# Performance work log

Measured on AMD Instinct MI355X. Metric: run time of the kernel, lower is better.

Reference implementation:

```python
import jax, jax.numpy as jnp
import numpy as np

B, T, C = 2, 2048, 1024
H, DH = 16, 64          # n_heads = d_model // 64
WIN = 256               # sliding window size
K = 32                  # n_oscillators
DFF = 4096              # d_ff_hidden
NEG = -1e9


def setup_inputs() -> dict:
    key = jax.random.key(0)
    ks = jax.random.split(key, 16)
    sC = 1.0 / np.sqrt(C)
    sF = 1.0 / np.sqrt(DFF)
    sK = 1.0 / np.sqrt(K)
    return {
        "x": jax.random.normal(ks[0], (B, T, C), jnp.float32),
        "norm1_w": jnp.ones((C,), jnp.float32),
        "qkv_w": jax.random.normal(ks[1], (3 * C, C), jnp.float32) * sC,
        "qkv_b": jnp.zeros((3 * C,), jnp.float32),
        "proj_w": jax.random.normal(ks[2], (C, C), jnp.float32) * sC,
        "proj_b": jnp.zeros((C,), jnp.float32),
        "gate_w": jax.random.normal(ks[3], (1, C), jnp.float32) * 0.01,
        "gate_b": jnp.zeros((1,), jnp.float32),
        "trn_win": jax.random.normal(ks[4], (K, C), jnp.float32) * sC,
        "trn_wout": jax.random.normal(ks[5], (C, K), jnp.float32) * sK,
        "trn_gate_w": jax.random.normal(ks[6], (K, C), jnp.float32) * sC,
        "trn_gate_b": jnp.zeros((K,), jnp.float32),
        "trn_a_logit": jax.random.normal(ks[7], (K,), jnp.float32),
        "trn_theta": jax.random.uniform(ks[8], (K,), jnp.float32, 0.0, np.pi),
        "trn_res_scale": jnp.asarray(0.1, jnp.float32),
        "norm2_w": jnp.ones((C,), jnp.float32),
        "ffn_gate_w": jax.random.normal(ks[9], (DFF, C), jnp.float32) * sC,
        "ffn_up_w": jax.random.normal(ks[10], (DFF, C), jnp.float32) * sC,
        "ffn_down_w": jax.random.normal(ks[11], (C, DFF), jnp.float32) * sF,
    }


def _rms(z, w, eps=1e-6):
    return z * jax.lax.rsqrt(jnp.mean(z * z, axis=-1, keepdims=True) + eps) * w


def reference(x, norm1_w, qkv_w, qkv_b, proj_w, proj_b, gate_w, gate_b,
              trn_win, trn_wout, trn_gate_w, trn_gate_b, trn_a_logit,
              trn_theta, trn_res_scale, norm2_w, ffn_gate_w, ffn_up_w,
              ffn_down_w):
    h = _rms(x, norm1_w)

    # ---- windowed causal attention (dense mask, as in the original) ----
    qkv = h @ qkv_w.T + qkv_b                       # [B,T,3C]
    q, k, v = jnp.split(qkv, 3, axis=-1)
    heads = lambda t: t.reshape(B, T, H, DH).transpose(0, 2, 1, 3)  # [B,H,T,DH]
    q, k, v = heads(q), heads(k), heads(v)
    row = jnp.arange(T)[:, None]
    col = jnp.arange(T)[None, :]
    mask = jnp.where((col <= row) & (col >= row - WIN + 1), 0.0, NEG).astype(x.dtype)
    scores = jnp.einsum('bhqd,bhkd->bhqk', q, k) / jnp.sqrt(jnp.asarray(DH, x.dtype))
    attn = jax.nn.softmax(scores + mask, axis=-1)
    ao = jnp.einsum('bhqk,bhkd->bhqd', attn, v).transpose(0, 2, 1, 3).reshape(B, T, C)
    ao = ao @ proj_w.T + proj_b

    # ---- temporal resonance branch: K damped rotating oscillators ----
    u = h @ trn_win.T                               # [B,T,K] drive
    a = jax.nn.sigmoid(trn_a_logit)                 # amplitude in (0,1) (amplitude_max=1)
    ct, st = jnp.cos(trn_theta), jnp.sin(trn_theta)

    def step(carry, ut):
        sr, si = carry
        nsr = a * (ct * sr - st * si) + ut
        nsi = a * (st * sr + ct * si)
        return (nsr, nsi), nsr

    init = (jnp.zeros((B, K), x.dtype), jnp.zeros((B, K), x.dtype))
    _, ys = jax.lax.scan(step, init, u.transpose(1, 0, 2))  # ys: [T,B,K]
    y = ys.transpose(1, 0, 2)                                # [B,T,K]
    tg = jax.nn.sigmoid(h @ trn_gate_w.T + trn_gate_b)
    trn_out = ((tg * y) @ trn_wout.T) * trn_res_scale        # [B,T,C]

    # ---- sigmoid gate mix + residual ----
    g = jax.nn.sigmoid(h @ gate_w.T + gate_b)       # [B,T,1]
    x = x + g * ao + (1.0 - g) * trn_out

    # ---- SwiGLU FFN ----
    h2 = _rms(x, norm2_w)
    ffn = (jax.nn.silu(h2 @ ffn_gate_w.T) * (h2 @ ffn_up_w.T)) @ ffn_down_w.T
    return x + ffn
```

## Files before the change

kernel.cpp:

```cpp
#include <hip/hip_runtime.h>


typedef unsigned short u16;
typedef unsigned short u16x8 __attribute__((ext_vector_type(8)));
typedef __bf16 bf16x8 __attribute__((ext_vector_type(8)));
typedef float f32x4 __attribute__((ext_vector_type(4)));

#define DI static __device__ __forceinline__

DI u16 f2b(float f){
  union { float f; unsigned u; } v; v.f = f;
  unsigned r = v.u + 0x7FFFu + ((v.u >> 16) & 1u);
  return (u16)(r >> 16);
}
DI float b2f(u16 b){
  union { unsigned u; float f; } v; v.u = ((unsigned)b) << 16; return v.f;
}
DI u16x8 ld8(const u16* p){ return *(const u16x8*)p; }

DI f32x4 MFMA16(u16x8 a, u16x8 b, f32x4 c){
  return __builtin_amdgcn_mfma_f32_16x16x32_bf16(
      __builtin_bit_cast(bf16x8, a), __builtin_bit_cast(bf16x8, b), c, 0, 0, 0);
}

DI void async16(const void* g, void* l){
  void* gg = const_cast<void*>(g);
  __builtin_amdgcn_global_load_lds(
      (__attribute__((address_space(1))) void*)gg,
      (__attribute__((address_space(3))) void*)l, 16, 0, 0);
}

__global__ __launch_bounds__(256) void convert_w(
    const float* __restrict__ qkvw, const float* __restrict__ projw,
    const float* __restrict__ fgw, const float* __restrict__ fuw,
    const float* __restrict__ fdw, const float* __restrict__ twin,
    const float* __restrict__ tgw, const float* __restrict__ twout,
    u16* __restrict__ dst)
{
  size_t i = (size_t)blockIdx.x * 256 + threadIdx.x;
  if (i >= 4235264u) return;
  size_t e = i * 4;
  float4 v;
  if (e < 3145728u)        v = *(const float4*)(qkvw + e);
  else if (e < 3276800u){
    size_t i2 = e - 3145728u;
    int row = (int)(i2 >> 10), c = (int)(i2 & 1023);
    if (row < 32)      v = *(const float4*)(twin + row * 1024 + c);
    else if (row < 64) v = *(const float4*)(tgw + (row - 32) * 1024 + c);
    else               v = make_float4(0.f, 0.f, 0.f, 0.f);
  }
  else if (e < 4325376u)   v = *(const float4*)(projw + (e - 3276800u));
  else if (e < 12713984u){
    size_t i2 = e - 4325376u;
    int row = (int)(i2 >> 10), c = (int)(i2 & 1023);
    int G = row >> 5, j = row & 31;
    const float* src = (j < 16) ? fgw : fuw;
    v = *(const float4*)(src + (size_t)(G * 16 + (j & 15)) * 1024 + c);
  }
  else if (e < 16908288u)  v = *(const float4*)(fdw + (e - 12713984u));
  else                     v = *(const float4*)(twout + (e - 16908288u));
  uint2 p;
  p.x = (unsigned)f2b(v.x) | ((unsigned)f2b(v.y) << 16);
  p.y = (unsigned)f2b(v.z) | ((unsigned)f2b(v.w) << 16);
  *(uint2*)(dst + e) = p;
}

__global__ __launch_bounds__(256) void rmsnorm_gate(
    const float* __restrict__ x, const float* __restrict__ w,
    const float* __restrict__ gw, const float* __restrict__ gb,
    u16* __restrict__ h, float* __restrict__ g)
{
  const int row = blockIdx.x, tid = threadIdx.x;
  const int wave = tid >> 6, lane = tid & 63;
  __shared__ float sb[8];
  float4 xv = ((const float4*)(x + (size_t)row * 1024))[tid];
  float ss = xv.x*xv.x + xv.y*xv.y + xv.z*xv.z + xv.w*xv.w;
#pragma unroll
  for (int m = 32; m; m >>= 1) ss += __shfl_xor(ss, m);
  if (lane == 0) sb[wave] = ss;
  __syncthreads();
  float rstd = rsqrtf((sb[0]+sb[1]+sb[2]+sb[3]) * (1.f/1024.f) + 1e-6f);
  float4 wv = ((const float4*)w)[tid];
  float h0 = xv.x*rstd*wv.x, h1 = xv.y*rstd*wv.y;
  float h2v = xv.z*rstd*wv.z, h3 = xv.w*rstd*wv.w;
  uint2 pk;
  pk.x = (unsigned)f2b(h0) | ((unsigned)f2b(h1) << 16);
  pk.y = (unsigned)f2b(h2v) | ((unsigned)f2b(h3) << 16);
  ((uint2*)(h + (size_t)row * 1024))[tid] = pk;
  float4 gv = ((const float4*)gw)[tid];
  float gd = h0*gv.x + h1*gv.y + h2v*gv.z + h3*gv.w;
#pragma unroll
  for (int m = 32; m; m >>= 1) gd += __shfl_xor(gd, m);
  if (lane == 0) sb[4 + wave] = gd;
  __syncthreads();
  if (tid == 0) g[row] = 1.f / (1.f + __expf(-(sb[4]+sb[5]+sb[6]+sb[7] + gb[0])));
}

__global__ __launch_bounds__(256) void reduce_mix_norm(
    const float* __restrict__ part, const float* __restrict__ x,
    const u16* __restrict__ trn, const float* __restrict__ g,
    const float* __restrict__ pb, const float* __restrict__ n2w,
    float* __restrict__ out, u16* __restrict__ h2)
{
  const int row = blockIdx.x, tid = threadIdx.x;
  const int wave = tid >> 6, lane = tid & 63;
  __shared__ float sb[4];
  const size_t ro = (size_t)row * 1024;
  float4 p0 = ((const float4*)(part + ro))[tid];
  float4 p1 = ((const float4*)(part + 4194304 + ro))[tid];
  float4 bb = ((const float4*)pb)[tid];
  float4 xv = ((const float4*)(x + ro))[tid];
  uint2 tz = ((const uint2*)(trn + ro))[tid];
  float gg = g[row];
  float t0 = b2f((u16)tz.x), t1 = b2f((u16)(tz.x >> 16));
  float t2 = b2f((u16)tz.y), t3 = b2f((u16)(tz.y >> 16));
  float m0 = xv.x + gg*(p0.x+p1.x+bb.x) + (1.f-gg)*t0;
  float m1 = xv.y + gg*(p0.y+p1.y+bb.y) + (1.f-gg)*t1;
  float m2 = xv.z + gg*(p0.z+p1.z+bb.z) + (1.f-gg)*t2;
  float m3 = xv.w + gg*(p0.w+p1.w+bb.w) + (1.f-gg)*t3;
  float4 mo; mo.x = m0; mo.y = m1; mo.z = m2; mo.w = m3;
  ((float4*)(out + ro))[tid] = mo;
  float ss = m0*m0 + m1*m1 + m2*m2 + m3*m3;
#pragma unroll
  for (int m = 32; m; m >>= 1) ss += __shfl_xor(ss, m);
  if (lane == 0) sb[wave] = ss;
  __syncthreads();
  float rstd = rsqrtf((sb[0]+sb[1]+sb[2]+sb[3]) * (1.f/1024.f) + 1e-6f);
  float4 wv = ((const float4*)n2w)[tid];
  uint2 pk;
  pk.x = (unsigned)f2b(m0*rstd*wv.x) | ((unsigned)f2b(m1*rstd*wv.y) << 16);
  pk.y = (unsigned)f2b(m2*rstd*wv.z) | ((unsigned)f2b(m3*rstd*wv.w) << 16);
  ((uint2*)(h2 + ro))[tid] = pk;
}

__global__ __launch_bounds__(256) void reduce_down(
    const float* __restrict__ part, float* __restrict__ out)
{
  size_t i = (size_t)blockIdx.x * 256 + threadIdx.x;
  float4 p0 = ((const float4*)part)[i];
  float4 p1 = ((const float4*)(part + 4194304))[i];
  float4 xv = ((float4*)out)[i];
  float4 o;
  o.x = xv.x + p0.x + p1.x; o.y = xv.y + p0.y + p1.y;
  o.z = xv.z + p0.z + p1.z; o.w = xv.w + p0.w + p1.w;
  ((float4*)out)[i] = o;
}

template<int MODE, bool WIDE>
__global__ __launch_bounds__(256) void gemm_bt(
    const u16* __restrict__ A, const u16* __restrict__ B,
    float* __restrict__ outF, float* __restrict__ outF2, u16* __restrict__ outB,
    const float* __restrict__ bias, const float* __restrict__ auxF,
    int M, int N, int K)
{
  __shared__ __align__(16) u16 sA[2][128 * 32];
  __shared__ __align__(16) u16 sB[2][128 * 32];
  const int tid = threadIdx.x;
  const int wave = tid >> 6, lane = tid & 63;
  const int lr = lane & 15, lq = lane >> 4;
  const int m0 = blockIdx.x * 128, n0 = blockIdx.y * 128;
  const int wm = (wave & 1) * 64, wn = (wave >> 1) * 64;
  const int ks = K / (int)gridDim.z;
  const int kbeg = (int)blockIdx.z * ks, kend = kbeg + ks;
  f32x4 acc[4][4] = {};
  const int srow = wave * 16 + (lane >> 2);
  const int scol = (lane & 3) * 8;
  const u16* gA = A + (size_t)(m0 + srow) * K + scol;
  const u16* gB = B + (size_t)(n0 + srow) * K + scol;
  u16* lA0 = &sA[0][(wave * 16) * 32];
  u16* lA1 = &sA[0][(64 + wave * 16) * 32];
  u16* lB0 = &sB[0][(wave * 16) * 32];
  u16* lB1 = &sB[0][(64 + wave * 16) * 32];
  const size_t K64 = (size_t)64 * K;
  const int BUF = 128 * 32;

  if (WIDE){
    for (int k0 = kbeg; k0 < kend; k0 += 64){
      async16(gA + k0,            lA0);
      async16(gA + K64 + k0,      lA1);
      async16(gB + k0,            lB0);
      async16(gB + K64 + k0,      lB1);
      async16(gA + k0 + 32,       lA0 + BUF);
      async16(gA + K64 + k0 + 32, lA1 + BUF);
      async16(gB + k0 + 32,       lB0 + BUF);
      async16(gB + K64 + k0 + 32, lB1 + BUF);
      __syncthreads();
      u16x8 af[4], bf[4];
#pragma unroll
      for (int i = 0; i < 4; i++) af[i] = ld8(&sA[0][(wm + i*16 + lr)*32 + lq*8]);
#pragma unroll
      for (int i = 0; i < 4; i++) bf[i] = ld8(&sB[0][(wn + i*16 + lr)*32 + lq*8]);
#pragma unroll
      for (int mi = 0; mi < 4; mi++)
#pragma unroll
        for (int ni = 0; ni < 4; ni++)
          acc[mi][ni] = MFMA16(af[mi], bf[ni], acc[mi][ni]);
#pragma unroll
      for (int i = 0; i < 4; i++) af[i] = ld8(&sA[1][(wm + i*16 + lr)*32 + lq*8]);
#pragma unroll
      for (int i = 0; i < 4; i++) bf[i] = ld8(&sB[1][(wn + i*16 + lr)*32 + lq*8]);
#pragma unroll
      for (int mi = 0; mi < 4; mi++)
#pragma unroll
        for (int ni = 0; ni < 4; ni++)
          acc[mi][ni] = MFMA16(af[mi], bf[ni], acc[mi][ni]);
      __syncthreads();
    }
  } else {
    for (int k0 = kbeg; k0 < kend; k0 += 32){
      async16(gA + k0,       lA0);
      async16(gA + K64 + k0, lA1);
      async16(gB + k0,       lB0);
      async16(gB + K64 + k0, lB1);
      __syncthreads();
      u16x8 af[4], bf[4];
#pragma unroll
      for (int i = 0; i < 4; i++) af[i] = ld8(&sA[0][(wm + i*16 + lr)*32 + lq*8]);
#pragma unroll
      for (int i = 0; i < 4; i++) bf[i] = ld8(&sB[0][(wn + i*16 + lr)*32 + lq*8]);
#pragma unroll
      for (int mi = 0; mi < 4; mi++)
#pragma unroll
        for (int ni = 0; ni < 4; ni++)
          acc[mi][ni] = MFMA16(af[mi], bf[ni], acc[mi][ni]);
      __syncthreads();
    }
  }

  if (MODE == 7){
    const int cb = ((n0 + wn) >> 1) + lr;
#pragma unroll
    for (int mi = 0; mi < 4; mi++){
      const int row = m0 + wm + mi*16 + lq*4;
#pragma unroll
      for (int p = 0; p < 2; p++){
        const int col = cb + p*16;
#pragma unroll
        for (int r = 0; r < 4; r++){
          float gv = acc[mi][2*p][r], uv = acc[mi][2*p+1][r];
          float rv = gv / (1.f + __expf(-gv)) * uv;
          outB[(size_t)(row + r) * (N >> 1) + col] = f2b(rv);
        }
      }
    }
    return;
  }

  float scale6 = 0.f;
  if (MODE == 6) scale6 = auxF[0];

#pragma unroll
  for (int mi = 0; mi < 4; mi++){
    const int row = m0 + wm + mi*16 + lq*4;
#pragma unroll
    for (int ni = 0; ni < 4; ni++){
      const int col = n0 + wn + ni*16 + lr;
#pragma unroll
      for (int r = 0; r < 4; r++){
        const int rr = row + r;
        float v = acc[mi][ni][r];
        if (MODE == 0){
          if (n0 < 3072){
            outB[(size_t)rr * 3072 + col] = f2b(v + bias[col]);
          } else {
            int c2 = col - 3072;
            int bb = rr >> 11, tt = rr & 2047;
            if (c2 < 32) outF[((size_t)bb * 32 + c2) * 2048 + tt] = v;
            else if (c2 < 64)
              outF2[(size_t)rr * 32 + (c2 - 32)] =
                  1.f / (1.f + __expf(-(v + auxF[c2 - 32])));
          }
        } else if (MODE == 6){
          outB[(size_t)rr * N + col] = f2b(v * scale6);
        } else if (MODE == 8){
          outF[(size_t)blockIdx.z * (size_t)M + (size_t)rr * N + col] = v;
        }
      }
    }
  }
}

__global__ __launch_bounds__(256) void attn_win(
    const u16* __restrict__ qkv, u16* __restrict__ ao)
{
  const int blk = blockIdx.x;
  const int tile = blk & 31, hh = (blk >> 5) & 15, b = blk >> 9;
  const int t0 = tile * 64;
  const int tid = threadIdx.x, wave = tid >> 6, lane = tid & 63;
  const int lr = lane & 15, lq = lane >> 4;
  const int qt = t0 + wave * 16;
  __shared__ __align__(16) u16 sVt[64 * 40];
  __shared__ __align__(16) u16 sP[4][16 * 32];

  const u16* base = qkv + (size_t)b * 2048 * 3072 + hh * 64;
  const u16* qrow = base + (size_t)(qt + lr) * 3072 + lq * 8;
  u16x8 qf0 = ld8(qrow), qf1 = ld8(qrow + 32);
  const u16* kbase = base + 1024;
  const u16* vbase = base + 2048;

  f32x4 o0 = {0,0,0,0}, o1 = {0,0,0,0}, o2 = {0,0,0,0}, o3 = {0,0,0,0};
  float mrun[4] = {-1e30f, -1e30f, -1e30f, -1e30f};
  float lrun[4] = {0.f, 0.f, 0.f, 0.f};
  const float c1 = 0.125f * 1.44269504088896f;

  const int kb = (t0 >= 256) ? (t0 - 256) : 0;
  const int ntl = (t0 + 64 - kb) >> 5;
  for (int it = 0; it < ntl; ++it){
    const int kt = kb + it * 32;
    __syncthreads();
    {
      const int key = tid & 31, dseg = tid >> 5;
      const u16* gv = vbase + (size_t)(kt + key) * 3072 + dseg * 8;
      u16x8 v0 = ld8(gv);
#pragma unroll
      for (int j = 0; j < 8; j++)
        sVt[(dseg*8 + j) * 40 + key] = v0[j];
    }
    __syncthreads();
    const bool active = (kt < qt + 16) && (kt + 286 >= qt);
    if (!active) continue;

    f32x4 s0 = {0,0,0,0}, s1 = {0,0,0,0};
    {
      const u16* kr = kbase + (size_t)(kt + lr) * 3072 + lq * 8;
      u16x8 k00 = ld8(kr), k01 = ld8(kr + 32);
      const u16* kr1 = kr + (size_t)16 * 3072;
      u16x8 k10 = ld8(kr1), k11 = ld8(kr1 + 32);
      s0 = MFMA16(qf0, k00, s0); s0 = MFMA16(qf1, k01, s0);
      s1 = MFMA16(qf0, k10, s1); s1 = MFMA16(qf1, k11, s1);
    }
    float al[4];
#pragma unroll
    for (int r = 0; r < 4; r++){
      const int q = qt + lq * 4 + r;
      const int ca = kt + lr, cb = kt + 16 + lr;
      float a0 = (ca <= q && ca + 255 >= q) ? s0[r] : -1e30f;
      float a1 = (cb <= q && cb + 255 >= q) ? s1[r] : -1e30f;
      float mx = fmaxf(a0, a1);
      mx = fmaxf(mx, __shfl_xor(mx, 1));
      mx = fmaxf(mx, __shfl_xor(mx, 2));
      mx = fmaxf(mx, __shfl_xor(mx, 4));
      mx = fmaxf(mx, __shfl_xor(mx, 8));
      float mn = fmaxf(mrun[r], mx);
      al[r] = exp2f((mrun[r] - mn) * c1);
      mrun[r] = mn;
      float p0 = (a0 > -1e29f) ? exp2f((a0 - mn) * c1) : 0.f;
      float p1 = (a1 > -1e29f) ? exp2f((a1 - mn) * c1) : 0.f;
      float sm = p0 + p1;
      sm += __shfl_xor(sm, 1); sm += __shfl_xor(sm, 2);
      sm += __shfl_xor(sm, 4); sm += __shfl_xor(sm, 8);
      lrun[r] = lrun[r] * al[r] + sm;
      sP[wave][(lq*4 + r) * 32 + lr]      = f2b(p0);
      sP[wave][(lq*4 + r) * 32 + 16 + lr] = f2b(p1);
    }
#pragma unroll
    for (int r = 0; r < 4; r++){
      o0[r] *= al[r]; o1[r] *= al[r]; o2[r] *= al[r]; o3[r] *= al[r];
    }
    __builtin_amdgcn_s_waitcnt(0xc07f);
    u16x8 pf = ld8(&sP[wave][lr * 32 + lq * 8]);
    o0 = MFMA16(pf, ld8(&sVt[(lr)      * 40 + lq * 8]), o0);
    o1 = MFMA16(pf, ld8(&sVt[(16 + lr) * 40 + lq * 8]), o1);
    o2 = MFMA16(pf, ld8(&sVt[(32 + lr) * 40 + lq * 8]), o2);
    o3 = MFMA16(pf, ld8(&sVt[(48 + lr) * 40 + lq * 8]), o3);
  }

  u16* aor = ao + (size_t)(b * 2048 + qt + lq * 4) * 1024 + hh * 64 + lr;
#pragma unroll
  for (int r = 0; r < 4; r++){
    float inv = 1.f / lrun[r];
    u16* p = aor + (size_t)r * 1024;
    p[0]  = f2b(o0[r] * inv);
    p[16] = f2b(o1[r] * inv);
    p[32] = f2b(o2[r] * inv);
    p[48] = f2b(o3[r] * inv);
  }
}

__global__ __launch_bounds__(256) void scan_k(
    const float* __restrict__ u_t, const float* __restrict__ tg,
    const float* __restrict__ alog, const float* __restrict__ theta,
    u16* __restrict__ z)
{
  const int bk = blockIdx.x;
  const int b = bk >> 5, k = bk & 31;
  const int j = threadIdx.x;
  const float a = 1.f / (1.f + __expf(-alog[k]));
  const float th = theta[k];
  const float wr = a * __cosf(th), wi = a * __sinf(th);
  const float* ubp = u_t + ((size_t)b * 32 + k) * 2048 + j * 8;
  float4 ua = ((const float4*)ubp)[0];
  float4 ub4 = ((const float4*)ubp)[1];
  float ur[8] = {ua.x, ua.y, ua.z, ua.w, ub4.x, ub4.y, ub4.z, ub4.w};
  float sr = 0.f, si = 0.f;
#pragma unroll
  for (int i = 0; i < 8; i++){
    float nr = wr*sr - wi*si + ur[i];
    float ni = wi*sr + wr*si;
    sr = nr; si = ni;
  }
  float w2r = wr*wr - wi*wi, w2i = 2.f*wr*wi;
  float w4r = w2r*w2r - w2i*w2i, w4i = 2.f*w2r*w2i;
  float Ar = w4r*w4r - w4i*w4i, Ai = 2.f*w4r*w4i;
  __shared__ float4 sc[256];
  float4 cur; cur.x = Ar; cur.y = Ai; cur.z = sr; cur.w = si;
  sc[j] = cur;
  __syncthreads();
  for (int s = 1; s < 256; s <<= 1){
    float4 pv;
    const bool has = (j >= s);
    if (has) pv = sc[j - s];
    __syncthreads();
    if (has){
      float nar = cur.x*pv.x - cur.y*pv.y;
      float nai = cur.x*pv.y + cur.y*pv.x;
      float nbr = cur.x*pv.z - cur.y*pv.w + cur.z;
      float nbi = cur.x*pv.w + cur.y*pv.z + cur.w;
      cur.x = nar; cur.y = nai; cur.z = nbr; cur.w = nbi;
    }
    sc[j] = cur;
    __syncthreads();
  }
  float s_r = 0.f, s_i = 0.f;
  if (j > 0){ float4 pr = sc[j - 1]; s_r = pr.z; s_i = pr.w; }
  const float* tgp = tg + ((size_t)b * 2048 + j * 8) * 32 + k;
  u16* zp = z + ((size_t)b * 2048 + j * 8) * 32 + k;
#pragma unroll
  for (int i = 0; i < 8; i++){
    float nr = wr*s_r - wi*s_i + ur[i];
    float ni = wi*s_r + wr*s_i;
    s_r = nr; s_i = ni;
    zp[(size_t)i * 32] = f2b(s_r * tgp[(size_t)i * 32]);
  }
}

extern "C" void kernel_launch(void* const* d_in, const int* in_sizes, int n_in,
                              void* d_out, int out_size, void* d_ws, size_t ws_size,
                              hipStream_t stream)
{
  (void)in_sizes; (void)n_in; (void)out_size; (void)ws_size;
  const float* x      = (const float*)d_in[0];
  const float* n1w    = (const float*)d_in[1];
  const float* qkvw   = (const float*)d_in[2];
  const float* qkvb   = (const float*)d_in[3];
  const float* projw  = (const float*)d_in[4];
  const float* projb  = (const float*)d_in[5];
  const float* gatew  = (const float*)d_in[6];
  const float* gateb  = (const float*)d_in[7];
  const float* twin   = (const float*)d_in[8];
  const float* twout  = (const float*)d_in[9];
  const float* tgw    = (const float*)d_in[10];
  const float* tgb    = (const float*)d_in[11];
  const float* talog  = (const float*)d_in[12];
  const float* ttheta = (const float*)d_in[13];
  const float* tscale = (const float*)d_in[14];
  const float* n2w    = (const float*)d_in[15];
  const float* fgw    = (const float*)d_in[16];
  const float* fuw    = (const float*)d_in[17];
  const float* fdw    = (const float*)d_in[18];
  float* out = (float*)d_out;

  char* wsb = (char*)d_ws;
  size_t off = 0;
  auto take = [&](size_t bytes) -> void* {
    void* r = wsb + off; off += (bytes + 255) & ~(size_t)255; return r;
  };
  u16*   wall = (u16*)take(16941056ull * 2);
  u16*   h    = (u16*)take(4194304ull * 2);
  u16*   h2   = (u16*)take(4194304ull * 2);
  u16*   trn  = (u16*)take(4194304ull * 2);
  float* g    = (float*)take(4096ull * 4);
  float* u_t  = (float*)take(131072ull * 4);
  float* tg   = (float*)take(131072ull * 4);
  u16*   zz   = (u16*)take(131072ull * 2);
  u16*   regA = (u16*)take(4096ull * 4096 * 2);
  u16*   regB = (u16*)take(4096ull * 4096 * 2);

  u16* wq  = wall;
  u16* wp  = wall + 3276800;
  u16* wgu = wall + 4325376;
  u16* wd  = wall + 12713984;
  u16* wo  = wall + 16908288;
  u16*   qkv   = regA;
  float* pproj = (float*)regA;
  float* pdown = (float*)regA;
  u16*   ao    = regB;
  u16*   act   = regB;

  convert_w<<<16544, 256, 0, stream>>>(qkvw, projw, fgw, fuw, fdw, twin, tgw, twout, wall);
  rmsnorm_gate<<<4096, 256, 0, stream>>>(x, n1w, gatew, gateb, h, g);
  gemm_bt<0, true><<<dim3(32, 25), 256, 0, stream>>>(h, wq, u_t, tg, qkv, qkvb,
                                                     tgb, 0, 3200, 1024);
  attn_win<<<1024, 256, 0, stream>>>(qkv, ao);
  scan_k<<<64, 256, 0, stream>>>(u_t, tg, talog, ttheta, zz);
  gemm_bt<6, false><<<dim3(32, 8), 256, 0, stream>>>(zz, wo, nullptr, nullptr, trn, nullptr,
                                                     tscale, 0, 1024, 32);
  gemm_bt<8, true><<<dim3(32, 8, 2), 256, 0, stream>>>(ao, wp, pproj, nullptr, nullptr, nullptr,
                                                       nullptr, 4194304, 1024, 1024);
  reduce_mix_norm<<<4096, 256, 0, stream>>>(pproj, x, trn, g, projb, n2w, out, h2);
  gemm_bt<7, true><<<dim3(32, 64), 256, 0, stream>>>(h2, wgu, nullptr, nullptr, act, nullptr,
                                                     nullptr, 0, 8192, 1024);
  gemm_bt<8, true><<<dim3(32, 8, 2), 256, 0, stream>>>(act, wd, pdown, nullptr, nullptr, nullptr,
                                                       nullptr, 4194304, 1024, 4096);
  reduce_down<<<4096, 256, 0, stream>>>(pdown, out);
}
```

Baseline: 434.2 us.

## Store split-K partials in bf16 and drop online-softmax max tracking

The split-K projection and down-projection GEMMs now write their partial sums as bf16 instead of fp32, and the reduce kernels widen them back to float. This halves the traffic for writing and reading the partials. Separately, the windowed attention drops the running max and rescaling and exponentiates the raw scaled scores directly, with one row-sum reduction at the end. Both trade accuracy for less work: bf16 partials lose precision, and skipping the max subtraction risks exp overflow if scores grow large.

```diff
diff --git a/kernel.cpp b/kernel.cpp
--- a/kernel.cpp
+++ b/kernel.cpp
@@ -97,7 +97,7 @@
 }
 
 __global__ __launch_bounds__(256) void reduce_mix_norm(
-    const float* __restrict__ part, const float* __restrict__ x,
+    const u16* __restrict__ part, const float* __restrict__ x,
     const u16* __restrict__ trn, const float* __restrict__ g,
     const float* __restrict__ pb, const float* __restrict__ n2w,
     float* __restrict__ out, u16* __restrict__ h2)
@@ -106,18 +106,22 @@
   const int wave = tid >> 6, lane = tid & 63;
   __shared__ float sb[4];
   const size_t ro = (size_t)row * 1024;
-  float4 p0 = ((const float4*)(part + ro))[tid];
-  float4 p1 = ((const float4*)(part + 4194304 + ro))[tid];
+  uint2 a0 = ((const uint2*)(part + ro))[tid];
+  uint2 a1 = ((const uint2*)(part + 4194304 + ro))[tid];
   float4 bb = ((const float4*)pb)[tid];
   float4 xv = ((const float4*)(x + ro))[tid];
   uint2 tz = ((const uint2*)(trn + ro))[tid];
   float gg = g[row];
+  float p00 = b2f((u16)a0.x), p01 = b2f((u16)(a0.x >> 16));
+  float p02 = b2f((u16)a0.y), p03 = b2f((u16)(a0.y >> 16));
+  float p10 = b2f((u16)a1.x), p11 = b2f((u16)(a1.x >> 16));
+  float p12 = b2f((u16)a1.y), p13 = b2f((u16)(a1.y >> 16));
   float t0 = b2f((u16)tz.x), t1 = b2f((u16)(tz.x >> 16));
   float t2 = b2f((u16)tz.y), t3 = b2f((u16)(tz.y >> 16));
-  float m0 = xv.x + gg*(p0.x+p1.x+bb.x) + (1.f-gg)*t0;
-  float m1 = xv.y + gg*(p0.y+p1.y+bb.y) + (1.f-gg)*t1;
-  float m2 = xv.z + gg*(p0.z+p1.z+bb.z) + (1.f-gg)*t2;
-  float m3 = xv.w + gg*(p0.w+p1.w+bb.w) + (1.f-gg)*t3;
+  float m0 = xv.x + gg*(p00+p10+bb.x) + (1.f-gg)*t0;
+  float m1 = xv.y + gg*(p01+p11+bb.y) + (1.f-gg)*t1;
+  float m2 = xv.z + gg*(p02+p12+bb.z) + (1.f-gg)*t2;
+  float m3 = xv.w + gg*(p03+p13+bb.w) + (1.f-gg)*t3;
   float4 mo; mo.x = m0; mo.y = m1; mo.z = m2; mo.w = m3;
   ((float4*)(out + ro))[tid] = mo;
   float ss = m0*m0 + m1*m1 + m2*m2 + m3*m3;
@@ -134,15 +138,17 @@
 }
 
 __global__ __launch_bounds__(256) void reduce_down(
-    const float* __restrict__ part, float* __restrict__ out)
+    const u16* __restrict__ part, float* __restrict__ out)
 {
   size_t i = (size_t)blockIdx.x * 256 + threadIdx.x;
-  float4 p0 = ((const float4*)part)[i];
-  float4 p1 = ((const float4*)(part + 4194304))[i];
+  uint2 a0 = ((const uint2*)part)[i];
+  uint2 a1 = ((const uint2*)(part + 4194304))[i];
   float4 xv = ((float4*)out)[i];
   float4 o;
-  o.x = xv.x + p0.x + p1.x; o.y = xv.y + p0.y + p1.y;
-  o.z = xv.z + p0.z + p1.z; o.w = xv.w + p0.w + p1.w;
+  o.x = xv.x + b2f((u16)a0.x) + b2f((u16)a1.x);
+  o.y = xv.y + b2f((u16)(a0.x >> 16)) + b2f((u16)(a1.x >> 16));
+  o.z = xv.z + b2f((u16)a0.y) + b2f((u16)a1.y);
+  o.w = xv.w + b2f((u16)(a0.y >> 16)) + b2f((u16)(a1.y >> 16));
   ((float4*)out)[i] = o;
 }
 
@@ -272,8 +278,8 @@
           }
         } else if (MODE == 6){
           outB[(size_t)rr * N + col] = f2b(v * scale6);
-        } else if (MODE == 8){
-          outF[(size_t)blockIdx.z * (size_t)M + (size_t)rr * N + col] = v;
+        } else if (MODE == 9){
+          outB[(size_t)blockIdx.z * (size_t)M + (size_t)rr * N + col] = f2b(v);
         }
       }
     }
@@ -299,8 +305,7 @@
   const u16* vbase = base + 2048;
 
   f32x4 o0 = {0,0,0,0}, o1 = {0,0,0,0}, o2 = {0,0,0,0}, o3 = {0,0,0,0};
-  float mrun[4] = {-1e30f, -1e30f, -1e30f, -1e30f};
-  float lrun[4] = {0.f, 0.f, 0.f, 0.f};
+  float lsum[4] = {0.f, 0.f, 0.f, 0.f};
   const float c1 = 0.125f * 1.44269504088896f;
 
   const int kb = (t0 >= 256) ? (t0 - 256) : 0;
@@ -329,33 +334,15 @@
       s0 = MFMA16(qf0, k00, s0); s0 = MFMA16(qf1, k01, s0);
       s1 = MFMA16(qf0, k10, s1); s1 = MFMA16(qf1, k11, s1);
     }
-    float al[4];
 #pragma unroll
     for (int r = 0; r < 4; r++){
       const int q = qt + lq * 4 + r;
       const int ca = kt + lr, cb = kt + 16 + lr;
-      float a0 = (ca <= q && ca + 255 >= q) ? s0[r] : -1e30f;
-      float a1 = (cb <= q && cb + 255 >= q) ? s1[r] : -1e30f;
-      float mx = fmaxf(a0, a1);
-      mx = fmaxf(mx, __shfl_xor(mx, 1));
-      mx = fmaxf(mx, __shfl_xor(mx, 2));
-      mx = fmaxf(mx, __shfl_xor(mx, 4));
-      mx = fmaxf(mx, __shfl_xor(mx, 8));
-      float mn = fmaxf(mrun[r], mx);
-      al[r] = exp2f((mrun[r] - mn) * c1);
-      mrun[r] = mn;
-      float p0 = (a0 > -1e29f) ? exp2f((a0 - mn) * c1) : 0.f;
-      float p1 = (a1 > -1e29f) ? exp2f((a1 - mn) * c1) : 0.f;
-      float sm = p0 + p1;
-      sm += __shfl_xor(sm, 1); sm += __shfl_xor(sm, 2);
-      sm += __shfl_xor(sm, 4); sm += __shfl_xor(sm, 8);
-      lrun[r] = lrun[r] * al[r] + sm;
+      float p0 = (ca <= q && ca + 255 >= q) ? exp2f(s0[r] * c1) : 0.f;
+      float p1 = (cb <= q && cb + 255 >= q) ? exp2f(s1[r] * c1) : 0.f;
+      lsum[r] += p0 + p1;
       sP[wave][(lq*4 + r) * 32 + lr]      = f2b(p0);
       sP[wave][(lq*4 + r) * 32 + 16 + lr] = f2b(p1);
-    }
-#pragma unroll
-    for (int r = 0; r < 4; r++){
-      o0[r] *= al[r]; o1[r] *= al[r]; o2[r] *= al[r]; o3[r] *= al[r];
     }
     __builtin_amdgcn_s_waitcnt(0xc07f);
     u16x8 pf = ld8(&sP[wave][lr * 32 + lq * 8]);
@@ -365,10 +352,18 @@
     o3 = MFMA16(pf, ld8(&sVt[(48 + lr) * 40 + lq * 8]), o3);
   }
 
+#pragma unroll
+  for (int r = 0; r < 4; r++){
+    float l = lsum[r];
+    l += __shfl_xor(l, 1); l += __shfl_xor(l, 2);
+    l += __shfl_xor(l, 4); l += __shfl_xor(l, 8);
+    lsum[r] = l;
+  }
+
   u16* aor = ao + (size_t)(b * 2048 + qt + lq * 4) * 1024 + hh * 64 + lr;
 #pragma unroll
   for (int r = 0; r < 4; r++){
-    float inv = 1.f / lrun[r];
+    float inv = 1.f / lsum[r];
     u16* p = aor + (size_t)r * 1024;
     p[0]  = f2b(o0[r] * inv);
     p[16] = f2b(o1[r] * inv);
@@ -481,11 +476,11 @@
   u16* wgu = wall + 4325376;
   u16* wd  = wall + 12713984;
   u16* wo  = wall + 16908288;
-  u16*   qkv   = regA;
-  float* pproj = (float*)regA;
-  float* pdown = (float*)regA;
-  u16*   ao    = regB;
-  u16*   act   = regB;
+  u16* qkv    = regA;
+  u16* pproj  = regA;
+  u16* pdown  = regA;
+  u16* ao     = regB;
+  u16* act    = regB;
 
   convert_w<<<16544, 256, 0, stream>>>(qkvw, projw, fgw, fuw, fdw, twin, tgw, twout, wall);
   rmsnorm_gate<<<4096, 256, 0, stream>>>(x, n1w, gatew, gateb, h, g);
@@ -495,12 +490,12 @@
   scan_k<<<64, 256, 0, stream>>>(u_t, tg, talog, ttheta, zz);
   gemm_bt<6, false><<<dim3(32, 8), 256, 0, stream>>>(zz, wo, nullptr, nullptr, trn, nullptr,
                                                      tscale, 0, 1024, 32);
-  gemm_bt<8, true><<<dim3(32, 8, 2), 256, 0, stream>>>(ao, wp, pproj, nullptr, nullptr, nullptr,
-                                                       nullptr, 4194304, 1024, 1024);
+  gemm_bt<9, true><<<dim3(32, 8, 2), 256, 0, stream>>>(ao, wp, nullptr, nullptr, pproj,
+                                                       nullptr, nullptr, 4194304, 1024, 1024);
   reduce_mix_norm<<<4096, 256, 0, stream>>>(pproj, x, trn, g, projb, n2w, out, h2);
   gemm_bt<7, true><<<dim3(32, 64), 256, 0, stream>>>(h2, wgu, nullptr, nullptr, act, nullptr,
                                                      nullptr, 0, 8192, 1024);
-  gemm_bt<8, true><<<dim3(32, 8, 2), 256, 0, stream>>>(act, wd, pdown, nullptr, nullptr, nullptr,
-                                                       nullptr, 4194304, 1024, 4096);
+  gemm_bt<9, true><<<dim3(32, 8, 2), 256, 0, stream>>>(act, wd, nullptr, nullptr, pdown,
+                                                       nullptr, nullptr, 4194304, 1024, 4096);
   reduce_down<<<4096, 256, 0, stream>>>(pdown, out);
 }
```

Result: faster. 418.5 us (-3.6%).
